# Performance work log

Hardware: AMD Instinct MI355X
Metric: run time of the kernel (lower is better)

## Reference

```python
import jax, jax.numpy as jnp
import numpy as np

B, N, L, E = 8, 2000, 128, 2048  # batch, nodes, local_size+1, ff_hidden_dim
PENALTY = 10.0


def setup_inputs() -> dict:
    key = jax.random.key(0)
    ks = jax.random.split(key, 8)
    dist = jax.random.uniform(ks[0], (B, N, N), jnp.float32) + 1e-3  # positive distances
    theta = jax.random.normal(ks[1], (B, N, N), jnp.float32)
    ins_feature0 = jax.random.normal(ks[2], (B, N, 1), jnp.float32)
    ins_feature1 = jax.random.normal(ks[3], (B, N, 1), jnp.float32)
    d_in = 2 * L + 2
    W1 = jax.random.normal(ks[4], (d_in, E), jnp.float32) * 0.02
    b1 = jnp.zeros((E,), jnp.float32)
    W2 = jax.random.normal(ks[5], (E, L), jnp.float32) * 0.02
    b2 = jnp.zeros((L,), jnp.float32)
    return {"theta": theta, "dist": dist, "ins_feature0": ins_feature0,
            "ins_feature1": ins_feature1, "W1": W1, "b1": b1, "W2": W2, "b2": b2}


def reference(theta, dist, ins_feature0, ins_feature1, W1, b1, W2, b2):
    k = W2.shape[1]  # local_size (L)
    # smallest-k along last dim, sorted ascending (torch.topk largest=False)
    neg_vals, idx = jax.lax.top_k(-dist, k)          # [B,N,L]
    sorted_dist = -neg_vals
    sorted_dist = sorted_dist / jnp.max(sorted_dist, axis=-1, keepdims=True)
    sorted_theta = jnp.take_along_axis(theta, idx, axis=-1)  # [B,N,L]
    x_in = jnp.concatenate([sorted_dist, sorted_theta, ins_feature0, ins_feature1], axis=-1)  # [B,N,2L+2]
    edge_emb = x_in @ W1 + b1                        # [B,N,E] (no nonlinearity, as in source)
    out = edge_emb @ W2 + b2 - sorted_dist           # [B,N,L]
    b_, n_, _ = dist.shape
    bi = jnp.arange(b_)[:, None, None]
    ni = jnp.arange(n_)[None, :, None]
    out_mat = jnp.full(dist.shape, PENALTY, dist.dtype).at[bi, ni, idx].set(out)
    return out_mat
```

## Files before the change

### kernel.cpp

```cpp
#include <hip/hip_runtime.h>
#include <hip/hip_bf16.h>

#define BN 8
#define NN 2000
#define LL 128
#define EE 2048
#define DIN 258
#define KPAD 264
#define NROWS (BN*NN)
#define PENALTY_V 10.0f
#define NBINS 256
#define CANDCAP 256
#define T0 0.092f
#define SPLITK 16
#define ECHUNK (EE/SPLITK)
#define RPB 4
#define AWORDS 4640

__global__ __launch_bounds__(256) void kA1(const float* __restrict__ W1,
                                           const float* __restrict__ b1,
                                           const float* __restrict__ W2,
                                           float* __restrict__ part) {
    __shared__ float As2[8][64];
    const int t = threadIdx.x;
    const int j = t & 127;
    const int half = t >> 7;
    const int rg = blockIdx.x >> 4;
    const int ks = blockIdx.x & 15;
    const int k0 = rg * 8;
    const int ebase = ks * ECHUNK;
    float acc[4] = {0.f, 0.f, 0.f, 0.f};
    for (int ec = ebase; ec < ebase + ECHUNK; ec += 64) {
        #pragma unroll
        for (int q = 0; q < 2; ++q) {
            int linear = q * 256 + t;
            int r8 = linear >> 6;
            int e  = linear & 63;
            int k  = k0 + r8;
            float v;
            if (k < DIN)       v = W1[k * EE + ec + e];
            else if (k == DIN) v = b1[ec + e];
            else               v = 0.0f;
            As2[r8][e] = v;
        }
        __syncthreads();
        #pragma unroll 8
        for (int e = 0; e < 64; ++e) {
            float w = W2[(ec + e) * LL + j];
            #pragma unroll
            for (int rr = 0; rr < 4; ++rr)
                acc[rr] += As2[half * 4 + rr][e] * w;
        }
        __syncthreads();
    }
    #pragma unroll
    for (int rr = 0; rr < 4; ++rr) {
        int k = k0 + half * 4 + rr;
        part[(size_t)ks * (KPAD * LL) + k * LL + j] = acc[rr];
    }
}

__global__ __launch_bounds__(256) void kA2(const float* __restrict__ part,
                                           const float* __restrict__ b2,
                                           float* __restrict__ Wc,
                                           float* __restrict__ bc) {
    const int i = blockIdx.x * 256 + threadIdx.x;
    float s = 0.f;
    #pragma unroll
    for (int q = 0; q < SPLITK; ++q) s += part[(size_t)q * (KPAD * LL) + i];
    const int k = i >> 7;
    const int j = i & 127;
    if (k == DIN)      { bc[j] = s + b2[j]; Wc[i] = 0.f; }
    else if (k > DIN)  { Wc[i] = 0.f; }
    else               { Wc[i] = s; }
}

__global__ __launch_bounds__(256) void kF(const float* __restrict__ dist,
                                          const float* __restrict__ theta,
                                          const float* __restrict__ f0,
                                          const float* __restrict__ f1,
                                          const float* __restrict__ Wc,
                                          const float* __restrict__ bc,
                                          float* __restrict__ out) {
    __shared__ __align__(16) unsigned int arena[AWORDS];
    const int t = threadIdx.x;
    const int lane = t & 63;
    const int w = t >> 6;
    const int row = blockIdx.x * RPB + w;

    unsigned int* hist = &arena[w * 768];
    unsigned long long* cand = (unsigned long long*)&arena[w * 768 + 256];
    float* xv = (float*)&arena[3072 + w * 264];
    int* oidx = (int*)&arena[4128 + w * 128];

    {
        uint4 z4 = {0u, 0u, 0u, 0u};
        *(uint4*)&hist[lane * 4] = z4;
        unsigned long long f1v = ~0ULL;
        #pragma unroll
        for (int q = 0; q < CANDCAP / 64; ++q) cand[lane + q * 64] = f1v;
    }

    unsigned int v[32];
    const int nv = (lane < 52) ? 32 : 28;
    {
        const uint4* drow4 = (const uint4*)(dist + (size_t)row * NN);
        #pragma unroll
        for (int q = 0; q < 8; ++q) {
            int qi = q * 64 + lane;
            if (qi < NN / 4) {
                uint4 a = drow4[qi];
                v[4 * q]     = a.x;
                v[4 * q + 1] = a.y;
                v[4 * q + 2] = a.z;
                v[4 * q + 3] = a.w;
            }
        }
    }

    float T = T0;
    unsigned int qm = 0u;
    #pragma unroll
    for (int k = 0; k < 32; ++k)
        if (k < nv && __uint_as_float(v[k]) <= T) qm |= (1u << k);
    int cnt = __builtin_popcount(qm);
    #pragma unroll
    for (int d = 1; d < 64; d <<= 1) cnt += __shfl_xor(cnt, d);

    if (cnt < LL || cnt > CANDCAP) {
        unsigned int lmax = 0u;
        #pragma unroll
        for (int k = 0; k < 32; ++k) if (k < nv) lmax = max(lmax, v[k]);
        #pragma unroll
        for (int d = 1; d < 64; d <<= 1) lmax = max(lmax, (unsigned int)__shfl_xor((int)lmax, d));
        float lo = 0.0f, hi = __uint_as_float(lmax);
        if (cnt < LL) lo = T; else hi = T;
        for (int it = 0; it < 32; ++it) {
            T = 0.5f * (lo + hi);
            unsigned int m = 0u;
            #pragma unroll
            for (int k = 0; k < 32; ++k)
                if (k < nv && __uint_as_float(v[k]) <= T) m |= (1u << k);
            int c = __builtin_popcount(m);
            #pragma unroll
            for (int d = 1; d < 64; d <<= 1) c += __shfl_xor(c, d);
            qm = m;
            if (c >= LL && c <= CANDCAP) break;
            if (c < LL) lo = T; else hi = T;
        }
    }
    const float scale2 = (float)(NBINS - 1) / T;

    #pragma unroll
    for (int k = 0; k < 32; ++k) {
        if ((qm >> k) & 1u) {
            float f = __uint_as_float(v[k]);
            int b = (int)(f * scale2);
            b = b > NBINS - 1 ? NBINS - 1 : b;
            atomicAdd(&hist[b], 1u);
        }
    }

    {
        uint4* h4 = (uint4*)&hist[lane * 4];
        uint4 a0 = *h4;
        unsigned int c[4] = {a0.x, a0.y, a0.z, a0.w};
        unsigned int loc[4], run = 0;
        #pragma unroll
        for (int k = 0; k < 4; ++k) { loc[k] = run; run += c[k]; }
        unsigned int inc = run;
        #pragma unroll
        for (int d = 1; d < 64; d <<= 1) {
            unsigned int o = (unsigned int)__shfl_up((int)inc, d);
            if (lane >= d) inc += o;
        }
        const unsigned int excl = inc - run;
        uint4 s0 = {excl + loc[0], excl + loc[1], excl + loc[2], excl + loc[3]};
        *h4 = s0;
    }

    #pragma unroll
    for (int k = 0; k < 32; ++k) {
        if ((qm >> k) & 1u) {
            unsigned int bits = v[k];
            float f = __uint_as_float(bits);
            int b = (int)(f * scale2);
            b = b > NBINS - 1 ? NBINS - 1 : b;
            unsigned int old = atomicAdd(&hist[b], 0x10000u);
            unsigned int slot = (old & 0xFFFFu) + (old >> 16);
            unsigned int idx = (unsigned int)((k >> 2) * 256 + lane * 4 + (k & 3));
            if (slot < (unsigned int)CANDCAP)
                cand[slot] = ((unsigned long long)bits << 32) | idx;
        }
    }

    {
        unsigned long long key_s[CANDCAP / 64];
        float th_s[CANDCAP / 64];
        #pragma unroll
        for (int s = 0; s < CANDCAP / 64; ++s) key_s[s] = cand[lane + s * 64];
        #pragma unroll
        for (int s = 0; s < CANDCAP / 64; ++s)
            if (key_s[s] != ~0ULL)
                th_s[s] = theta[(size_t)row * NN + (unsigned int)key_s[s]];
        #pragma unroll
        for (int s = 0; s < CANDCAP / 64; ++s) {
            unsigned long long key = key_s[s];
            if (key != ~0ULL) {
                unsigned int bits = (unsigned int)(key >> 32);
                unsigned int idx  = (unsigned int)key;
                float f = __uint_as_float(bits);
                int b = (int)(f * scale2);
                b = b > NBINS - 1 ? NBINS - 1 : b;
                unsigned int word = hist[b];
                unsigned int start = word & 0xFFFFu;
                unsigned int end = start + (word >> 16);
                if (end > (unsigned int)CANDCAP) end = (unsigned int)CANDCAP;
                unsigned int r = start;
                for (unsigned int jj = start; jj < end; ++jj) r += (cand[jj] < key);
                if (r < (unsigned int)LL) {
                    xv[r] = f;
                    xv[LL + r] = th_s[s];
                    oidx[r] = (int)idx;
                }
            }
        }
    }

    {
        const float rdm = 1.0f / xv[LL - 1];
        xv[lane] *= rdm;
        xv[lane + 64] *= rdm;
        if (lane == 0) {
            xv[256] = f0[row];
            xv[257] = f1[row];
            #pragma unroll
            for (int z = DIN; z < KPAD; ++z) xv[z] = 0.0f;
        }
    }

    __syncthreads();

    const int j = t & 127;
    const int rp = t >> 7;
    const float* x0 = (const float*)&arena[3072 + (2 * rp) * 264];
    const float* x1 = (const float*)&arena[3072 + (2 * rp + 1) * 264];
    float acc0 = bc[j] - x0[j];
    float acc1 = bc[j] - x1[j];
    #pragma unroll 2
    for (int k = 0; k < KPAD; k += 8) {
        float w0 = Wc[(k + 0) * LL + j];
        float w1 = Wc[(k + 1) * LL + j];
        float w2 = Wc[(k + 2) * LL + j];
        float w3 = Wc[(k + 3) * LL + j];
        float w4 = Wc[(k + 4) * LL + j];
        float w5 = Wc[(k + 5) * LL + j];
        float w6 = Wc[(k + 6) * LL + j];
        float w7 = Wc[(k + 7) * LL + j];
        float4 xa0 = *(const float4*)&x0[k];
        float4 xa1 = *(const float4*)&x0[k + 4];
        float4 xb0 = *(const float4*)&x1[k];
        float4 xb1 = *(const float4*)&x1[k + 4];
        acc0 += xa0.x * w0; acc1 += xb0.x * w0;
        acc0 += xa0.y * w1; acc1 += xb0.y * w1;
        acc0 += xa0.z * w2; acc1 += xb0.z * w2;
        acc0 += xa0.w * w3; acc1 += xb0.w * w3;
        acc0 += xa1.x * w4; acc1 += xb1.x * w4;
        acc0 += xa1.y * w5; acc1 += xb1.y * w5;
        acc0 += xa1.z * w6; acc1 += xb1.z * w6;
        acc0 += xa1.w * w7; acc1 += xb1.w * w7;
    }
    const int oi0 = ((const int*)&arena[4128 + (2 * rp) * 128])[j];
    const int oi1 = ((const int*)&arena[4128 + (2 * rp + 1) * 128])[j];

    {
        const float4 pen4 = {PENALTY_V, PENALTY_V, PENALTY_V, PENALTY_V};
        float4* ob = (float4*)(out + (size_t)blockIdx.x * RPB * NN);
        #pragma unroll
        for (int q = 0; q < 8; ++q) {
            int i = q * 256 + t;
            if (i < RPB * (NN / 4)) ob[i] = pen4;
        }
        __syncthreads();
        out[((size_t)blockIdx.x * RPB + 2 * rp) * NN + oi0] = acc0;
        out[((size_t)blockIdx.x * RPB + 2 * rp + 1) * NN + oi1] = acc1;
    }
}

extern "C" void kernel_launch(void* const* d_in, const int* in_sizes, int n_in,
                              void* d_out, int out_size, void* d_ws, size_t ws_size,
                              hipStream_t stream) {
    const float* theta = (const float*)d_in[0];
    const float* dist  = (const float*)d_in[1];
    const float* f0    = (const float*)d_in[2];
    const float* f1    = (const float*)d_in[3];
    const float* W1    = (const float*)d_in[4];
    const float* b1    = (const float*)d_in[5];
    const float* W2    = (const float*)d_in[6];
    const float* b2    = (const float*)d_in[7];
    float* out = (float*)d_out;

    char* ws = (char*)d_ws;
    float* Wc   = (float*)ws;
    float* bc   = (float*)(ws + 135168);
    float* part = (float*)(ws + 135680);

    kA1<<<33 * SPLITK, 256, 0, stream>>>(W1, b1, W2, part);
    kA2<<<(KPAD * LL) / 256, 256, 0, stream>>>(part, b2, Wc, bc);
    kF<<<NROWS / RPB, 256, 0, stream>>>(dist, theta, f0, f1, Wc, bc, out);
}
```

Measured before the change: 120.1 us.

## Make final GEMV per-wavefront and issue penalty fill early to drop block barriers

Each wavefront now handles its own row all the way through: the shared arena is split per wave, the GEMV computes 128 outputs per row with two columns per lane, and the block-wide __syncthreads calls are removed. The penalty fill of the output row is moved up to right after the distance load so it overlaps the top-k selection. Before the scatter, an s_waitcnt vmcnt(0) is relied on to order the fill stores ahead of the scattered writes within the wave. In exchange, Wc loads are no longer shared between two rows per thread, so global and L1 traffic for Wc per row roughly doubles.

```diff
diff --git a/kernel.cpp b/kernel.cpp
--- a/kernel.cpp
+++ b/kernel.cpp
@@ -15,7 +15,7 @@
 #define SPLITK 16
 #define ECHUNK (EE/SPLITK)
 #define RPB 4
-#define AWORDS 4640
+#define WWORDS 1160
 
 __global__ __launch_bounds__(256) void kA1(const float* __restrict__ W1,
                                            const float* __restrict__ b1,
@@ -82,16 +82,16 @@
                                           const float* __restrict__ Wc,
                                           const float* __restrict__ bc,
                                           float* __restrict__ out) {
-    __shared__ __align__(16) unsigned int arena[AWORDS];
+    __shared__ __align__(16) unsigned int arena[RPB][WWORDS];
     const int t = threadIdx.x;
     const int lane = t & 63;
     const int w = t >> 6;
     const int row = blockIdx.x * RPB + w;
 
-    unsigned int* hist = &arena[w * 768];
-    unsigned long long* cand = (unsigned long long*)&arena[w * 768 + 256];
-    float* xv = (float*)&arena[3072 + w * 264];
-    int* oidx = (int*)&arena[4128 + w * 128];
+    unsigned int* hist = &arena[w][0];
+    unsigned long long* cand = (unsigned long long*)&arena[w][256];
+    float* xv = (float*)&arena[w][768];
+    int* oidx = (int*)&arena[w][1032];
 
     {
         uint4 z4 = {0u, 0u, 0u, 0u};
@@ -126,6 +126,16 @@
     int cnt = __builtin_popcount(qm);
     #pragma unroll
     for (int d = 1; d < 64; d <<= 1) cnt += __shfl_xor(cnt, d);
+
+    {
+        const float4 pen4 = {PENALTY_V, PENALTY_V, PENALTY_V, PENALTY_V};
+        float4* orow = (float4*)(out + (size_t)row * NN);
+        #pragma unroll
+        for (int q = 0; q < 8; ++q) {
+            int qi = q * 64 + lane;
+            if (qi < NN / 4) orow[qi] = pen4;
+        }
+    }
 
     if (cnt < LL || cnt > CANDCAP) {
         unsigned int lmax = 0u;
@@ -239,52 +249,43 @@
         }
     }
 
-    __syncthreads();
-
-    const int j = t & 127;
-    const int rp = t >> 7;
-    const float* x0 = (const float*)&arena[3072 + (2 * rp) * 264];
-    const float* x1 = (const float*)&arena[3072 + (2 * rp + 1) * 264];
-    float acc0 = bc[j] - x0[j];
-    float acc1 = bc[j] - x1[j];
+    float acc_a = bc[lane] - xv[lane];
+    float acc_b = bc[lane + 64] - xv[lane + 64];
     #pragma unroll 2
     for (int k = 0; k < KPAD; k += 8) {
-        float w0 = Wc[(k + 0) * LL + j];
-        float w1 = Wc[(k + 1) * LL + j];
-        float w2 = Wc[(k + 2) * LL + j];
-        float w3 = Wc[(k + 3) * LL + j];
-        float w4 = Wc[(k + 4) * LL + j];
-        float w5 = Wc[(k + 5) * LL + j];
-        float w6 = Wc[(k + 6) * LL + j];
-        float w7 = Wc[(k + 7) * LL + j];
-        float4 xa0 = *(const float4*)&x0[k];
-        float4 xa1 = *(const float4*)&x0[k + 4];
-        float4 xb0 = *(const float4*)&x1[k];
-        float4 xb1 = *(const float4*)&x1[k + 4];
-        acc0 += xa0.x * w0; acc1 += xb0.x * w0;
-        acc0 += xa0.y * w1; acc1 += xb0.y * w1;
-        acc0 += xa0.z * w2; acc1 += xb0.z * w2;
-        acc0 += xa0.w * w3; acc1 += xb0.w * w3;
-        acc0 += xa1.x * w4; acc1 += xb1.x * w4;
-        acc0 += xa1.y * w5; acc1 += xb1.y * w5;
-        acc0 += xa1.z * w6; acc1 += xb1.z * w6;
-        acc0 += xa1.w * w7; acc1 += xb1.w * w7;
-    }
-    const int oi0 = ((const int*)&arena[4128 + (2 * rp) * 128])[j];
-    const int oi1 = ((const int*)&arena[4128 + (2 * rp + 1) * 128])[j];
-
-    {
-        const float4 pen4 = {PENALTY_V, PENALTY_V, PENALTY_V, PENALTY_V};
-        float4* ob = (float4*)(out + (size_t)blockIdx.x * RPB * NN);
-        #pragma unroll
-        for (int q = 0; q < 8; ++q) {
-            int i = q * 256 + t;
-            if (i < RPB * (NN / 4)) ob[i] = pen4;
-        }
-        __syncthreads();
-        out[((size_t)blockIdx.x * RPB + 2 * rp) * NN + oi0] = acc0;
-        out[((size_t)blockIdx.x * RPB + 2 * rp + 1) * NN + oi1] = acc1;
-    }
+        float4 xk0 = *(const float4*)&xv[k];
+        float4 xk1 = *(const float4*)&xv[k + 4];
+        float wa0 = Wc[(k + 0) * LL + lane];
+        float wb0 = Wc[(k + 0) * LL + lane + 64];
+        float wa1 = Wc[(k + 1) * LL + lane];
+        float wb1 = Wc[(k + 1) * LL + lane + 64];
+        float wa2 = Wc[(k + 2) * LL + lane];
+        float wb2 = Wc[(k + 2) * LL + lane + 64];
+        float wa3 = Wc[(k + 3) * LL + lane];
+        float wb3 = Wc[(k + 3) * LL + lane + 64];
+        float wa4 = Wc[(k + 4) * LL + lane];
+        float wb4 = Wc[(k + 4) * LL + lane + 64];
+        float wa5 = Wc[(k + 5) * LL + lane];
+        float wb5 = Wc[(k + 5) * LL + lane + 64];
+        float wa6 = Wc[(k + 6) * LL + lane];
+        float wb6 = Wc[(k + 6) * LL + lane + 64];
+        float wa7 = Wc[(k + 7) * LL + lane];
+        float wb7 = Wc[(k + 7) * LL + lane + 64];
+        acc_a += xk0.x * wa0; acc_b += xk0.x * wb0;
+        acc_a += xk0.y * wa1; acc_b += xk0.y * wb1;
+        acc_a += xk0.z * wa2; acc_b += xk0.z * wb2;
+        acc_a += xk0.w * wa3; acc_b += xk0.w * wb3;
+        acc_a += xk1.x * wa4; acc_b += xk1.x * wb4;
+        acc_a += xk1.y * wa5; acc_b += xk1.y * wb5;
+        acc_a += xk1.z * wa6; acc_b += xk1.z * wb6;
+        acc_a += xk1.w * wa7; acc_b += xk1.w * wb7;
+    }
+    const int oa = oidx[lane];
+    const int ob = oidx[lane + 64];
+
+    asm volatile("s_waitcnt vmcnt(0)" ::: "memory");
+    out[(size_t)row * NN + oa] = acc_a;
+    out[(size_t)row * NN + ob] = acc_b;
 }
 
 extern "C" void kernel_launch(void* const* d_in, const int* in_sizes, int n_in,
```

Measured after the change: 164.5 us. 36.9% more time.
